# Optimization experiments

Measured on AMD Instinct MI355X. Metric: run time of the kernel, lower is better.

## Reference

```python
import jax, jax.numpy as jnp
import numpy as np

INPUT_SIZE = 256
HIDDEN_SIZE = 256
BATCH = 64
SEQ_LEN = 2048


def setup_inputs() -> dict:
    key = jax.random.key(0)
    ks = jax.random.split(key, 5)
    s_ih = 1.0 / np.sqrt(HIDDEN_SIZE)
    x = jax.random.normal(ks[0], (BATCH, SEQ_LEN, INPUT_SIZE), dtype=jnp.float32)
    W_ih = jax.random.uniform(ks[1], (4 * HIDDEN_SIZE, INPUT_SIZE), minval=-s_ih, maxval=s_ih, dtype=jnp.float32)
    W_hh = jax.random.uniform(ks[2], (4 * HIDDEN_SIZE, HIDDEN_SIZE), minval=-s_ih, maxval=s_ih, dtype=jnp.float32)
    b_ih = jax.random.uniform(ks[3], (4 * HIDDEN_SIZE,), minval=-s_ih, maxval=s_ih, dtype=jnp.float32)
    b_hh = jax.random.uniform(ks[4], (4 * HIDDEN_SIZE,), minval=-s_ih, maxval=s_ih, dtype=jnp.float32)
    return {"x": x, "W_ih": W_ih, "W_hh": W_hh, "b_ih": b_ih, "b_hh": b_hh}


def _lstm_forward(x, W_ih, W_hh, b_ih, b_hh):
    B, S, _ = x.shape
    H = W_hh.shape[1]
    # Precompute input projections for all timesteps in one big GEMM: [B,S,4H]
    x_proj = jnp.einsum('bsi,gi->bsg', x, W_ih) + b_ih + b_hh

    def step(carry, xp_t):
        h, c = carry
        gates = xp_t + h @ W_hh.T  # [B, 4H]
        i, f, g, o = jnp.split(gates, 4, axis=-1)
        i = jax.nn.sigmoid(i)
        f = jax.nn.sigmoid(f)
        g = jnp.tanh(g)
        o = jax.nn.sigmoid(o)
        c = f * c + i * g
        h = o * jnp.tanh(c)
        return (h, c), h

    h0 = jnp.zeros((B, H), dtype=x.dtype)
    c0 = jnp.zeros((B, H), dtype=x.dtype)
    (h, c), outs = jax.lax.scan(step, (h0, c0), jnp.swapaxes(x_proj, 0, 1))
    outputs = jnp.swapaxes(outs, 0, 1)  # [B, S, H]
    return outputs, (h, c)


def reference(x, W_ih, W_hh, b_ih, b_hh):
    return _lstm_forward(x, W_ih, W_hh, b_ih, b_hh)
```

## Files before the change

kernel.cpp:

```cpp
#include <hip/hip_runtime.h>
#include <hip/hip_bf16.h>

#define BATCH 64
#define SEQ   2048
#define ISZ   256
#define H     256
#define G4    1024
#define M_TOT (BATCH*SEQ)

typedef _Float16 half8  __attribute__((ext_vector_type(8)));
typedef _Float16 half2v __attribute__((ext_vector_type(2)));
typedef float    f32x4  __attribute__((ext_vector_type(4)));

union U32H2 { unsigned int u; half2v h; };
static __device__ __forceinline__ half2v u2h(unsigned int u){ U32H2 x; x.u = u; return x.h; }

#if __has_builtin(__builtin_amdgcn_fdot2)
#define FDOT2(w,hp,acc) __builtin_amdgcn_fdot2(u2h(w), u2h(hp), (acc), false)
#else
static __device__ __forceinline__ float fdot2_sw(unsigned int w, unsigned int hp, float acc){
  half2v wv = u2h(w), hv = u2h(hp);
  return acc + (float)wv[0]*(float)hv[0] + (float)wv[1]*(float)hv[1];
}
#define FDOT2(w,hp,acc) fdot2_sw((w),(hp),(acc))
#endif

__global__ __launch_bounds__(256) void prep_kernel(
    const float* __restrict__ Wih, const float* __restrict__ Whh,
    const float* __restrict__ bih, const float* __restrict__ bhh,
    _Float16* __restrict__ Wihf, unsigned int* __restrict__ Wpk,
    float* __restrict__ bias) {
  const int idx = blockIdx.x * 256 + threadIdx.x;
  Wihf[idx] = (_Float16)Wih[idx];
  if (idx < 131072) {
    const int t = idx & 1023, k2 = idx >> 10;
    U32H2 p;
    p.h[0] = (_Float16)Whh[t*256 + 2*k2];
    p.h[1] = (_Float16)Whh[t*256 + 2*k2 + 1];
    Wpk[idx] = p.u;
  }
  if (idx < 1024) bias[idx] = bih[idx] + bhh[idx];
}

#define BM 128
#define BN 128
#define BK 32
#define LDA 40

__global__ __launch_bounds__(256) void xproj_gemm(
    const float* __restrict__ X, const _Float16* __restrict__ Wihf,
    const float* __restrict__ bias, _Float16* __restrict__ XP) {
  __shared__ _Float16 As[BM*LDA];
  __shared__ _Float16 Bs[BN*LDA];
  const int tid  = threadIdx.x;
  const int m0   = blockIdx.x * BM;
  const int n0   = blockIdx.y * BN;
  const int lane = tid & 63;
  const int w    = tid >> 6;
  const int wm   = w & 1, wn = w >> 1;
  const int row  = tid >> 1, hlf = tid & 1;

  f32x4 acc[4][4];
  #pragma unroll
  for (int mi = 0; mi < 4; ++mi)
    #pragma unroll
    for (int ni = 0; ni < 4; ++ni)
      acc[mi][ni] = (f32x4){0.f, 0.f, 0.f, 0.f};

  for (int kt = 0; kt < ISZ/BK; ++kt) {
    const int k0 = kt * BK;
    __syncthreads();
    {
      const float4* pa = (const float4*)(X + (size_t)(m0+row)*ISZ + k0 + hlf*16);
      float4 f0 = pa[0], f1 = pa[1], f2 = pa[2], f3 = pa[3];
      half8 h0, h1;
      h0[0]=(_Float16)f0.x; h0[1]=(_Float16)f0.y; h0[2]=(_Float16)f0.z; h0[3]=(_Float16)f0.w;
      h0[4]=(_Float16)f1.x; h0[5]=(_Float16)f1.y; h0[6]=(_Float16)f1.z; h0[7]=(_Float16)f1.w;
      h1[0]=(_Float16)f2.x; h1[1]=(_Float16)f2.y; h1[2]=(_Float16)f2.z; h1[3]=(_Float16)f2.w;
      h1[4]=(_Float16)f3.x; h1[5]=(_Float16)f3.y; h1[6]=(_Float16)f3.z; h1[7]=(_Float16)f3.w;
      *(half8*)&As[row*LDA + hlf*16]     = h0;
      *(half8*)&As[row*LDA + hlf*16 + 8] = h1;
      const half8* pb = (const half8*)(Wihf + (size_t)(n0+row)*ISZ + k0 + hlf*16);
      half8 b0 = pb[0], b1 = pb[1];
      *(half8*)&Bs[row*LDA + hlf*16]     = b0;
      *(half8*)&Bs[row*LDA + hlf*16 + 8] = b1;
    }
    __syncthreads();
    const int kch = (lane >> 4) * 8;
    const int rm  = wm*64 + (lane & 15);
    const int rn  = wn*64 + (lane & 15);
    half8 af[4], bf[4];
    #pragma unroll
    for (int i = 0; i < 4; ++i) {
      af[i] = *(const half8*)&As[(rm + i*16)*LDA + kch];
      bf[i] = *(const half8*)&Bs[(rn + i*16)*LDA + kch];
    }
    #pragma unroll
    for (int mi = 0; mi < 4; ++mi)
      #pragma unroll
      for (int ni = 0; ni < 4; ++ni)
        acc[mi][ni] = __builtin_amdgcn_mfma_f32_16x16x32_f16(af[mi], bf[ni], acc[mi][ni], 0, 0, 0);
  }
  const int col = lane & 15, qr = (lane >> 4) * 4;
  #pragma unroll
  for (int ni = 0; ni < 4; ++ni) {
    const int n  = n0 + wn*64 + ni*16 + col;
    const float bs = bias[n];
    #pragma unroll
    for (int mi = 0; mi < 4; ++mi) {
      #pragma unroll
      for (int r = 0; r < 4; ++r) {
        const int m = m0 + wm*64 + mi*16 + qr + r;
        XP[(size_t)m*G4 + n] = (_Float16)(acc[mi][ni][r] + bs);
      }
    }
  }
}

#define NR  100
#define NLQ 7

__global__ __launch_bounds__(1024) void lstm_scan(
    const _Float16* __restrict__ XP, const unsigned int* __restrict__ Wpk,
    float* __restrict__ out) {
  __shared__ uint4 wlds[NLQ*1024];
  __shared__ float act[G4];
  __shared__ unsigned int h2[H/2];
  const int t = threadIdx.x;
  const int b = blockIdx.x;

  unsigned int wreg[NR];
  #pragma unroll
  for (int i = 0; i < NR; ++i) wreg[i] = Wpk[i*1024 + t];
  #pragma unroll
  for (int q = 0; q < NLQ; ++q) {
    uint4 v;
    v.x = Wpk[(NR + 4*q + 0)*1024 + t];
    v.y = Wpk[(NR + 4*q + 1)*1024 + t];
    v.z = Wpk[(NR + 4*q + 2)*1024 + t];
    v.w = Wpk[(NR + 4*q + 3)*1024 + t];
    wlds[q*1024 + t] = v;
  }
  if (t < H/2) h2[t] = 0u;
  float c = 0.f;
  const _Float16* xb = XP + (size_t)b*SEQ*G4 + t;
  float xcur = (float)xb[0];
  float* outb = out + (size_t)b*SEQ*H;
  __syncthreads();

  #pragma unroll 1
  for (int s = 0; s < SEQ; ++s) {
    const int sn = (s + 1 < SEQ) ? (s + 1) : s;
    const _Float16 xnext = xb[(size_t)sn * G4];

    float acc0 = xcur, acc1 = 0.f;
    #pragma unroll
    for (int q = 0; q < NR/4; ++q) {
      uint4 hq = *(const uint4*)(h2 + 4*q);
      acc0 = FDOT2(wreg[4*q+0], hq.x, acc0);
      acc1 = FDOT2(wreg[4*q+1], hq.y, acc1);
      acc0 = FDOT2(wreg[4*q+2], hq.z, acc0);
      acc1 = FDOT2(wreg[4*q+3], hq.w, acc1);
    }
    #pragma unroll
    for (int q = 0; q < NLQ; ++q) {
      uint4 hq = *(const uint4*)(h2 + NR + 4*q);
      uint4 wv = wlds[q*1024 + t];
      acc0 = FDOT2(wv.x, hq.x, acc0);
      acc1 = FDOT2(wv.y, hq.y, acc1);
      acc0 = FDOT2(wv.z, hq.z, acc0);
      acc1 = FDOT2(wv.w, hq.w, acc1);
    }
    const float gate = acc0 + acc1;
    float a;
    if (t < 512 || t >= 768) a = 1.f / (1.f + __expf(-gate));
    else                     a = 2.f / (1.f + __expf(-2.f*gate)) - 1.f;
    act[t] = a;
    __syncthreads();
    if (t < H) {
      const float gi = act[t], gf = act[H+t], gg = act[2*H+t], go = act[3*H+t];
      c = gf*c + gi*gg;
      const float th = 2.f / (1.f + __expf(-2.f*c)) - 1.f;
      const float h = go*th;
      outb[(size_t)s*H + t] = h;
      ((_Float16*)h2)[t] = (_Float16)h;
      if (s == SEQ-1) {
        out[(size_t)BATCH*SEQ*H + (size_t)b*H + t] = h;
        out[(size_t)BATCH*SEQ*H + (size_t)BATCH*H + (size_t)b*H + t] = c;
      }
    }
    xcur = (float)xnext;
    __syncthreads();
  }
}

extern "C" void kernel_launch(void* const* d_in, const int* in_sizes, int n_in,
                              void* d_out, int out_size, void* d_ws, size_t ws_size,
                              hipStream_t stream) {
  const float* x   = (const float*)d_in[0];
  const float* Wih = (const float*)d_in[1];
  const float* Whh = (const float*)d_in[2];
  const float* bih = (const float*)d_in[3];
  const float* bhh = (const float*)d_in[4];
  float* out = (float*)d_out;

  char* ws = (char*)d_ws;
  const size_t XP_BYTES = (size_t)M_TOT * G4 * sizeof(_Float16);
  _Float16*     XPp  = (_Float16*)ws;
  _Float16*     Wihf = (_Float16*)(ws + XP_BYTES);
  unsigned int* Wpk  = (unsigned int*)(ws + XP_BYTES + 524288);
  float*        bias = (float*)(ws + XP_BYTES + 1048576);

  prep_kernel<<<dim3(1024),            dim3(256),  0, stream>>>(Wih, Whh, bih, bhh, Wihf, Wpk, bias);
  xproj_gemm <<<dim3(M_TOT/BM, G4/BN), dim3(256),  0, stream>>>(x, Wihf, bias, XPp);
  lstm_scan  <<<dim3(BATCH),           dim3(1024), 0, stream>>>(XPp, Wpk, out);
}
```

Baseline: 4.249 ms.

## Split gate rows across thread pairs, stream tail weights from global with DPP reduce

Repacks W_hh so each adjacent thread pair computes two gate rows, each thread covering half the hidden dimension, with partial sums combined via a DPP xor-1 swap. Most weights stay in registers; the remaining chunks are loaded from global memory each timestep instead of LDS, and the h buffer is padded so the two halves use different LDS banks. The aim is to remove the LDS weight reads and bank conflicts, at the cost of per-step global/L2 load latency on the serial recurrence and an extra cross-lane reduction.

```diff
diff --git a/kernel.cpp b/kernel.cpp
--- a/kernel.cpp
+++ b/kernel.cpp
@@ -14,6 +14,7 @@
 
 union U32H2 { unsigned int u; half2v h; };
 static __device__ __forceinline__ half2v u2h(unsigned int u){ U32H2 x; x.u = u; return x.h; }
+union F32I { float f; int i; };
 
 #if __has_builtin(__builtin_amdgcn_fdot2)
 #define FDOT2(w,hp,acc) __builtin_amdgcn_fdot2(u2h(w), u2h(hp), (acc), false)
@@ -24,6 +25,16 @@
 }
 #define FDOT2(w,hp,acc) fdot2_sw((w),(hp),(acc))
 #endif
+
+static __device__ __forceinline__ float dpp_xor1(float v){
+#if __has_builtin(__builtin_amdgcn_update_dpp)
+  F32I a; a.f = v;
+  F32I r; r.i = __builtin_amdgcn_update_dpp(0, a.i, 0xB1 , 0xF, 0xF, true);
+  return r.f;
+#else
+  return __shfl_xor(v, 1, 64);
+#endif
+}
 
 __global__ __launch_bounds__(256) void prep_kernel(
     const float* __restrict__ Wih, const float* __restrict__ Whh,
@@ -33,10 +44,12 @@
   const int idx = blockIdx.x * 256 + threadIdx.x;
   Wihf[idx] = (_Float16)Wih[idx];
   if (idx < 131072) {
-    const int t = idx & 1023, k2 = idx >> 10;
+    const int cc = idx & 3, t = (idx >> 2) & 1023, q = idx >> 12;
+    const int row = (t & ~1) | (q >> 4);
+    const int pi  = (t & 1) * 64 + (q & 15) * 4 + cc;
     U32H2 p;
-    p.h[0] = (_Float16)Whh[t*256 + 2*k2];
-    p.h[1] = (_Float16)Whh[t*256 + 2*k2 + 1];
+    p.h[0] = (_Float16)Whh[row*256 + 2*pi];
+    p.h[1] = (_Float16)Whh[row*256 + 2*pi + 1];
     Wpk[idx] = p.u;
   }
   if (idx < 1024) bias[idx] = bih[idx] + bhh[idx];
@@ -117,35 +130,26 @@
   }
 }
 
-#define NR  100
-#define NLQ 7
-
 __global__ __launch_bounds__(1024) void lstm_scan(
-    const _Float16* __restrict__ XP, const unsigned int* __restrict__ Wpk,
+    const _Float16* __restrict__ XP, const uint4* __restrict__ WQ,
     float* __restrict__ out) {
-  __shared__ uint4 wlds[NLQ*1024];
   __shared__ float act[G4];
-  __shared__ unsigned int h2[H/2];
+  __shared__ __align__(16) unsigned int h2[136];
   const int t = threadIdx.x;
   const int b = blockIdx.x;
 
-  unsigned int wreg[NR];
-  #pragma unroll
-  for (int i = 0; i < NR; ++i) wreg[i] = Wpk[i*1024 + t];
-  #pragma unroll
-  for (int q = 0; q < NLQ; ++q) {
-    uint4 v;
-    v.x = Wpk[(NR + 4*q + 0)*1024 + t];
-    v.y = Wpk[(NR + 4*q + 1)*1024 + t];
-    v.z = Wpk[(NR + 4*q + 2)*1024 + t];
-    v.w = Wpk[(NR + 4*q + 3)*1024 + t];
-    wlds[q*1024 + t] = v;
-  }
-  if (t < H/2) h2[t] = 0u;
+  uint4 wq0[16], wq1[8];
+  #pragma unroll
+  for (int q = 0; q < 16; ++q) wq0[q] = WQ[q*1024 + t];
+  #pragma unroll
+  for (int j = 0; j < 8; ++j)  wq1[j] = WQ[(16+j)*1024 + t];
+
+  if (t < 136) h2[t] = 0u;
   float c = 0.f;
   const _Float16* xb = XP + (size_t)b*SEQ*G4 + t;
   float xcur = (float)xb[0];
   float* outb = out + (size_t)b*SEQ*H;
+  const unsigned int* hb = h2 + (t & 1) * 72;
   __syncthreads();
 
   #pragma unroll 1
@@ -153,25 +157,27 @@
     const int sn = (s + 1 < SEQ) ? (s + 1) : s;
     const _Float16 xnext = xb[(size_t)sn * G4];
 
-    float acc0 = xcur, acc1 = 0.f;
-    #pragma unroll
-    for (int q = 0; q < NR/4; ++q) {
-      uint4 hq = *(const uint4*)(h2 + 4*q);
-      acc0 = FDOT2(wreg[4*q+0], hq.x, acc0);
-      acc1 = FDOT2(wreg[4*q+1], hq.y, acc1);
-      acc0 = FDOT2(wreg[4*q+2], hq.z, acc0);
-      acc1 = FDOT2(wreg[4*q+3], hq.w, acc1);
-    }
-    #pragma unroll
-    for (int q = 0; q < NLQ; ++q) {
-      uint4 hq = *(const uint4*)(h2 + NR + 4*q);
-      uint4 wv = wlds[q*1024 + t];
-      acc0 = FDOT2(wv.x, hq.x, acc0);
-      acc1 = FDOT2(wv.y, hq.y, acc1);
-      acc0 = FDOT2(wv.z, hq.z, acc0);
-      acc1 = FDOT2(wv.w, hq.w, acc1);
-    }
-    const float gate = acc0 + acc1;
+    uint4 sA = WQ[24*1024 + t];
+    uint4 sB = WQ[25*1024 + t];
+
+    float a0 = 0.f, a1 = 0.f, b0 = 0.f, b1 = 0.f;
+    #pragma unroll
+    for (int q = 0; q < 16; ++q) {
+      uint4 hq = *(const uint4*)(hb + 4*q);
+      uint4 w0 = wq0[q];
+      a0 = FDOT2(w0.x, hq.x, a0); a1 = FDOT2(w0.y, hq.y, a1);
+      a0 = FDOT2(w0.z, hq.z, a0); a1 = FDOT2(w0.w, hq.w, a1);
+      uint4 w1;
+      if (q < 8) { w1 = wq1[q]; }
+      else       { w1 = sA; sA = sB; if (q < 14) sB = WQ[(18+q)*1024 + t]; }
+      b0 = FDOT2(w1.x, hq.x, b0); b1 = FDOT2(w1.y, hq.y, b1);
+      b0 = FDOT2(w1.z, hq.z, b0); b1 = FDOT2(w1.w, hq.w, b1);
+    }
+    const float p0 = a0 + a1, p1 = b0 + b1;
+    const float g0 = p0 + dpp_xor1(p0);
+    const float g1 = p1 + dpp_xor1(p1);
+    const float gate = ((t & 1) ? g1 : g0) + xcur;
+
     float a;
     if (t < 512 || t >= 768) a = 1.f / (1.f + __expf(-gate));
     else                     a = 2.f / (1.f + __expf(-2.f*gate)) - 1.f;
@@ -183,7 +189,7 @@
       const float th = 2.f / (1.f + __expf(-2.f*c)) - 1.f;
       const float h = go*th;
       outb[(size_t)s*H + t] = h;
-      ((_Float16*)h2)[t] = (_Float16)h;
+      ((_Float16*)h2)[t + (t >= 128 ? 16 : 0)] = (_Float16)h;
       if (s == SEQ-1) {
         out[(size_t)BATCH*SEQ*H + (size_t)b*H + t] = h;
         out[(size_t)BATCH*SEQ*H + (size_t)BATCH*H + (size_t)b*H + t] = c;
@@ -213,5 +219,5 @@
 
   prep_kernel<<<dim3(1024),            dim3(256),  0, stream>>>(Wih, Whh, bih, bhh, Wihf, Wpk, bias);
   xproj_gemm <<<dim3(M_TOT/BM, G4/BN), dim3(256),  0, stream>>>(x, Wihf, bias, XPp);
-  lstm_scan  <<<dim3(BATCH),           dim3(1024), 0, stream>>>(XPp, Wpk, out);
-}
+  lstm_scan  <<<dim3(BATCH),           dim3(1024), 0, stream>>>(XPp, (const uint4*)Wpk, out);
+}
```

Measured after the change: 7.597 ms. 78.8% more time.
